# Kernel optimization log

Measured on AMD Instinct MI355X. Metric: run time of the kernel, lower is better.

Reference implementation:

```python
import jax, jax.numpy as jnp
import numpy as np

TEMPERATURE = 0.07
EPS = 1e-12  # F.normalize eps


def _l2norm(x):
    n = jnp.linalg.norm(x, axis=-1, keepdims=True)
    return x / jnp.maximum(n, EPS)


def setup_inputs() -> dict:
    key = jax.random.key(0)
    k1, k2 = jax.random.split(key)
    B, T, H = 16, 512, 1024
    h_source = jax.random.normal(k1, (B, T, H), dtype=jnp.float32)
    h_target = jax.random.normal(k2, (B, T, H), dtype=jnp.float32)
    src_mask = jnp.ones((B, T), dtype=bool)
    tgt_mask = jnp.ones((B, T), dtype=bool)
    return {"h_source": h_source, "h_target": h_target,
            "src_mask": src_mask, "tgt_mask": tgt_mask}


def reference(h_source, h_target, src_mask, tgt_mask):
    # Masks are all-True and B*T == max_samples, so boolean selection == reshape
    # and the random subsampling branch is never taken (deterministic path).
    H = h_source.shape[-1]
    h_s = h_source.reshape(-1, H).astype(jnp.float32)          # (N, H)
    h_t = jax.lax.stop_gradient(h_target.reshape(-1, H)).astype(jnp.float32)  # detached

    h_s_norm = _l2norm(h_s)                                     # (N, H)
    h_t_norm = _l2norm(h_t)                                     # (M, H)
    sim = h_s_norm @ h_t_norm.T                                 # (N, M) cosine sim

    pos_idx = jnp.argmax(sim, axis=1)                           # == topk_idx[:, 0]
    logits = sim / TEMPERATURE
    # cross-entropy with pos_idx labels (stable log-softmax)
    logp = jax.nn.log_softmax(logits, axis=1)
    l_contrastive = -jnp.mean(jnp.take_along_axis(logp, pos_idx[:, None], axis=1)[:, 0])

    # contextual consistency: adjacent source tokens' NN embeddings should align
    nn_embeds = h_t_norm[pos_idx]                               # (N, H)
    nn_sim = jnp.sum(nn_embeds[:-1] * nn_embeds[1:], axis=-1)   # (N-1,)
    l_contextual = 1.0 - jnp.mean(nn_sim)

    return (l_contrastive, l_contextual)
```

## Files before the change

kernel.cpp:

```cpp
#include <hip/hip_runtime.h>
#include <hip/hip_bf16.h>
#include <stdint.h>


#define HDIM 1024
#define NROW 8192
#define TEMP_INV (1.0f / 0.07f)

typedef __attribute__((ext_vector_type(4))) float float4v;
typedef __attribute__((ext_vector_type(2))) float float2v;
typedef __attribute__((ext_vector_type(4))) int   int4v;
typedef __attribute__((ext_vector_type(8))) int   int8v;

#define SN_OFF   ((size_t)0)
#define TN_OFF   ((size_t)8388608)
#define TR_OFF   ((size_t)16777216)
#define SUM_OFF  ((size_t)25165824)
#define PMX_OFF  (SUM_OFF + 32768)
#define ACC_OFF  (PMX_OFF + 65536)
#define CNT_OFF  (ACC_OFF + 64)

static __device__ __forceinline__ void gload_lds16(const void* gptr, void* lptr) {
    __builtin_amdgcn_global_load_lds(
        (const __attribute__((address_space(1))) void*)gptr,
        (__attribute__((address_space(3))) void*)(uintptr_t)(uint32_t)(uintptr_t)lptr,
        16, 0, 0);
}

static __device__ __forceinline__ float fp8dot4(unsigned a, unsigned b) {
    float2v al = __builtin_amdgcn_cvt_pk_f32_fp8((int)a, false);
    float2v ah = __builtin_amdgcn_cvt_pk_f32_fp8((int)a, true);
    float2v bl = __builtin_amdgcn_cvt_pk_f32_fp8((int)b, false);
    float2v bh = __builtin_amdgcn_cvt_pk_f32_fp8((int)b, true);
    return al[0]*bl[0] + al[1]*bl[1] + ah[0]*bh[0] + ah[1]*bh[1];
}

__global__ __launch_bounds__(256)
void norm_kernel(const float* __restrict__ hs, const float* __restrict__ ht,
                 char* __restrict__ Sn, char* __restrict__ Tn, char* __restrict__ Tr,
                 float* __restrict__ sumexp, unsigned long long* __restrict__ pmax,
                 float* __restrict__ acc, unsigned* __restrict__ cnt) {
    const int b = blockIdx.x;
    const int t = threadIdx.x;
    const int wave = t >> 6, lane = t & 63;
    const bool isT = (b >= 512);
    const int g = isT ? (b - 512) : b;
    const float* in = (isT ? ht : hs) + (size_t)g * 16 * HDIM;
    char* outTiled = (isT ? Tn : Sn) + (size_t)g * 16384;

    __shared__ float sq[16][256];
    __shared__ float sscale[16];

    float4v v[16];
    #pragma unroll
    for (int i = 0; i < 16; ++i) {
        v[i] = ((const float4v*)in)[i * 256 + t];
        sq[i][t] = v[i][0]*v[i][0] + v[i][1]*v[i][1] + v[i][2]*v[i][2] + v[i][3]*v[i][3];
    }
    __syncthreads();
    #pragma unroll
    for (int j = 0; j < 4; ++j) {
        const int ri = wave * 4 + j;
        float s = sq[ri][lane] + sq[ri][lane + 64] + sq[ri][lane + 128] + sq[ri][lane + 192];
        #pragma unroll
        for (int off = 1; off < 64; off <<= 1) s += __shfl_xor(s, off);
        if (lane == 0) sscale[ri] = 1.0f / fmaxf(sqrtf(s), 1e-12f);
    }
    __syncthreads();

    char* tiled = (char*)sq;
    const int koff = (t >> 5) * 2048 + ((t >> 2) & 1) * 1024
                   + ((t >> 3) & 3) * 256 + (t & 3) * 4;
    #pragma unroll
    for (int i = 0; i < 16; ++i) {
        const float sc = sscale[i];
        int d = __builtin_amdgcn_cvt_pk_fp8_f32(v[i][0]*sc, v[i][1]*sc, 0, false);
        d     = __builtin_amdgcn_cvt_pk_fp8_f32(v[i][2]*sc, v[i][3]*sc, d, true);
        *(int*)(tiled + koff + i * 16) = d;
        if (isT) ((int*)(Tr + (size_t)(g * 16 + i) * HDIM))[t] = d;
    }
    __syncthreads();
    #pragma unroll
    for (int j = 0; j < 4; ++j)
        ((uint4*)outTiled)[j * 256 + t] = ((const uint4*)tiled)[j * 256 + t];

    if (!isT && t < 16) { sumexp[b * 16 + t] = 0.f; pmax[b * 16 + t] = 0ull; }
    if (b == 0 && t == 16) { acc[0] = 0.f; acc[1] = 0.f; *cnt = 0u; }
}

__global__ __launch_bounds__(256)
__attribute__((amdgpu_waves_per_eu(3, 3)))
void flash_kernel(const char* __restrict__ Sn, const char* __restrict__ Tn,
                  float* __restrict__ sumexp, unsigned long long* __restrict__ pmax) {
    __shared__ float pbSe[128];
    __shared__ unsigned long long pbPk[128];
    const int t = threadIdx.x;
    const int wave = t >> 6, lane = t & 63;
    const int quad = lane >> 4, l16 = lane & 15;

    const int bid = (int)blockIdx.x;
    const int xcd = bid & 7;
    const int idx = bid >> 3;
    const int oct = idx >> 6;
    const int w   = idx & 63;
    const int rbase = (oct * 8 + (w & 7)) * 128;
    const int cbase = (xcd * 8 + (w >> 3)) * 128;

    const int wr = wave & 1, wc = wave >> 1;
    const int wm = wr * 64, wn = wc * 64;

    int vA[4], vB[4];
    #pragma unroll
    for (int u = 0; u < 4; ++u) {
        vA[u] = (rbase / 16 + wr * 4 + u) * 16384 + lane * 16;
        vB[u] = (cbase / 16 + wc * 4 + u) * 16384 + lane * 16;
    }

    float4v acc[4][4];
    #pragma unroll
    for (int i = 0; i < 4; ++i)
        #pragma unroll
        for (int j = 0; j < 4; ++j) acc[i][j] = (float4v){0.f, 0.f, 0.f, 0.f};
    const int usc = 0x7f7f7f7f;

    #pragma unroll 1
    for (int kb = 0; kb < 8; ++kb) {
        int4v alo[4], ahi[4], blo[4], bhi[4];
        #pragma unroll
        for (int u = 0; u < 4; ++u) {
            alo[u] = *(const int4v*)(Sn + vA[u]);
            ahi[u] = *(const int4v*)(Sn + vA[u] + 1024);
        }
        #pragma unroll
        for (int u = 0; u < 4; ++u) {
            blo[u] = *(const int4v*)(Tn + vB[u]);
            bhi[u] = *(const int4v*)(Tn + vB[u] + 1024);
        }
        #pragma unroll
        for (int u = 0; u < 4; ++u) { vA[u] += 2048; vB[u] += 2048; }

        int8v af[4];
        #pragma unroll
        for (int i = 0; i < 4; ++i)
            af[i] = __builtin_shufflevector(alo[i], ahi[i], 0, 1, 2, 3, 4, 5, 6, 7);
        #pragma unroll
        for (int j = 0; j < 4; ++j) {
            int8v bf = __builtin_shufflevector(blo[j], bhi[j], 0, 1, 2, 3, 4, 5, 6, 7);
            #pragma unroll
            for (int i = 0; i < 4; ++i)
                acc[i][j] = __builtin_amdgcn_mfma_scale_f32_16x16x128_f8f6f4(
                    af[i], bf, acc[i][j], 0, 0, 0, usc, 0, usc);
        }
    }

    float se_v[4][4]; unsigned long long pk_v[4][4];
    #pragma unroll
    for (int i = 0; i < 4; ++i) {
        #pragma unroll
        for (int r = 0; r < 4; ++r) {
            float se = 0.f; float mx = -2.f; int mi = 0x7fffffff;
            #pragma unroll
            for (int j = 0; j < 4; ++j) {
                float v = acc[i][j][r];
                se += __expf(v * TEMP_INV);
                int col = cbase + wn + j * 16 + l16;
                if (v > mx || (v == mx && col < mi)) { mx = v; mi = col; }
            }
            #pragma unroll
            for (int off = 1; off < 16; off <<= 1) {
                se += __shfl_xor(se, off);
                float om = __shfl_xor(mx, off);
                int oi = __shfl_xor(mi, off);
                if (om > mx || (om == mx && oi < mi)) { mx = om; mi = oi; }
            }
            se_v[i][r] = se;
            pk_v[i][r] = ((unsigned long long)__float_as_uint(mx + 2.0f) << 32)
                         | (unsigned long long)(0xffffffffu - (unsigned)mi);
        }
    }
    if (wave < 2 && l16 == 0) {
        #pragma unroll
        for (int i = 0; i < 4; ++i)
            #pragma unroll
            for (int r = 0; r < 4; ++r) {
                int rl = wm + i * 16 + quad * 4 + r;
                pbSe[rl] = se_v[i][r]; pbPk[rl] = pk_v[i][r];
            }
    }
    __syncthreads();
    if (wave >= 2 && l16 == 0) {
        #pragma unroll
        for (int i = 0; i < 4; ++i)
            #pragma unroll
            for (int r = 0; r < 4; ++r) {
                int rl = wm + i * 16 + quad * 4 + r;
                float se = se_v[i][r] + pbSe[rl];
                unsigned long long pk = pk_v[i][r];
                unsigned long long po = pbPk[rl];
                if (po > pk) pk = po;
                atomicAdd(&sumexp[rbase + rl], se);
                atomicMax(&pmax[rbase + rl], pk);
            }
    }
}

__global__ __launch_bounds__(256)
void tail_kernel(const float* __restrict__ sumexp,
                 const unsigned long long* __restrict__ pmax,
                 const char* __restrict__ Tr,
                 float* __restrict__ acc, unsigned* __restrict__ cnt,
                 float* __restrict__ out) {
    const int blk = blockIdx.x;
    const int t = threadIdx.x, wave = t >> 6, lane = t & 63;

    if (wave == 0) {
        int r = blk * 32 + (lane & 31);
        unsigned long long p = pmax[r];
        float mx = __uint_as_float((unsigned)(p >> 32)) - 2.0f;
        float loss = logf(sumexp[r]) - mx * TEMP_INV;
        #pragma unroll
        for (int off = 1; off < 32; off <<= 1) loss += __shfl_xor(loss, off);
        if (lane == 0) atomicAdd(acc + 0, loss);
    }

    float s = 0.f;
    #pragma unroll
    for (int it = 0; it < 8; ++it) {
        int g = blk * 32 + wave * 8 + it;
        if (g < NROW - 1) {
            unsigned long long pa = pmax[g], pb = pmax[g + 1];
            int ia = (int)(0xffffffffu - (unsigned)(pa & 0xffffffffu));
            int ib = (int)(0xffffffffu - (unsigned)(pb & 0xffffffffu));
            uint4 va = ((const uint4*)(Tr + (size_t)ia * HDIM))[lane];
            uint4 vb = ((const uint4*)(Tr + (size_t)ib * HDIM))[lane];
            s += fp8dot4(va.x, vb.x) + fp8dot4(va.y, vb.y)
               + fp8dot4(va.z, vb.z) + fp8dot4(va.w, vb.w);
        }
    }
    #pragma unroll
    for (int off = 1; off < 64; off <<= 1) s += __shfl_xor(s, off);
    __shared__ float red[4];
    if (lane == 0) red[wave] = s;
    __syncthreads();
    if (t == 0) atomicAdd(acc + 1, red[0] + red[1] + red[2] + red[3]);

    __threadfence();
    __shared__ unsigned done;
    if (t == 0) done = atomicAdd(cnt, 1u);
    __syncthreads();
    if (t == 0 && done == 255u) {
        float l0 = atomicAdd(acc + 0, 0.0f);
        float l1 = atomicAdd(acc + 1, 0.0f);
        out[0] = l0 / (float)NROW;
        out[1] = 1.0f - l1 / (float)(NROW - 1);
    }
}

extern "C" void kernel_launch(void* const* d_in, const int* in_sizes, int n_in,
                              void* d_out, int out_size, void* d_ws, size_t ws_size,
                              hipStream_t stream) {
    const float* hs = (const float*)d_in[0];
    const float* ht = (const float*)d_in[1];
    char* ws = (char*)d_ws;
    char* Sn = ws + SN_OFF;
    char* Tn = ws + TN_OFF;
    char* Tr = ws + TR_OFF;
    float* sumexp = (float*)(ws + SUM_OFF);
    unsigned long long* pmax = (unsigned long long*)(ws + PMX_OFF);
    float* acc = (float*)(ws + ACC_OFF);
    unsigned* cnt = (unsigned*)(ws + CNT_OFF);
    float* out = (float*)d_out;

    norm_kernel<<<1024, 256, 0, stream>>>(hs, ht, Sn, Tn, Tr, sumexp, pmax, acc, cnt);
    flash_kernel<<<4096, 256, 0, stream>>>(Sn, Tn, sumexp, pmax);
    tail_kernel<<<256, 256, 0, stream>>>(sumexp, pmax, Tr, acc, cnt, out);
}
```

Before: 263.8 us.

## Stage FP8 GEMM operands through double-buffered LDS with async global-to-LDS loads

The flash kernel previously loaded the A and B fp8 tiles straight from global memory into registers on every k-step, and each wave re-read data that other waves also needed. It now copies each k-slab into a double-buffered LDS tile with global_load_lds, prefetching two stages ahead, and feeds the MFMAs from LDS. Barriers and vmcnt waits sequence the buffers, and MFMA issue priority is raised. This cuts redundant global traffic and hides load latency, at the cost of 64KB of LDS per block and occupancy lowered from 3 to 2 waves per EU.

```diff
diff --git a/kernel.cpp b/kernel.cpp
--- a/kernel.cpp
+++ b/kernel.cpp
@@ -89,11 +89,14 @@
 }
 
 __global__ __launch_bounds__(256)
-__attribute__((amdgpu_waves_per_eu(3, 3)))
+__attribute__((amdgpu_waves_per_eu(2, 2)))
 void flash_kernel(const char* __restrict__ Sn, const char* __restrict__ Tn,
                   float* __restrict__ sumexp, unsigned long long* __restrict__ pmax) {
+    __shared__ __align__(16) char As[2][16384];
+    __shared__ __align__(16) char Bs[2][16384];
     __shared__ float pbSe[128];
     __shared__ unsigned long long pbPk[128];
+
     const int t = threadIdx.x;
     const int wave = t >> 6, lane = t & 63;
     const int quad = lane >> 4, l16 = lane & 15;
@@ -109,12 +112,25 @@
     const int wr = wave & 1, wc = wave >> 1;
     const int wm = wr * 64, wn = wc * 64;
 
-    int vA[4], vB[4];
+    int offA[4], offB[4];
     #pragma unroll
     for (int u = 0; u < 4; ++u) {
-        vA[u] = (rbase / 16 + wr * 4 + u) * 16384 + lane * 16;
-        vB[u] = (cbase / 16 + wc * 4 + u) * 16384 + lane * 16;
-    }
+        int ua = wave * 4 + u;
+        offA[u] = (rbase / 16 + (ua >> 1)) * 16384 + (ua & 1) * 1024 + lane * 16;
+        offB[u] = (cbase / 16 + (ua >> 1)) * 16384 + (ua & 1) * 1024 + lane * 16;
+    }
+
+    auto STAGE = [&](int s) {
+        const int ks = s * 2048;
+        char* Ad = As[s & 1];
+        char* Bd = Bs[s & 1];
+        #pragma unroll
+        for (int u = 0; u < 4; ++u)
+            gload_lds16(Sn + offA[u] + ks, Ad + (wave * 4 + u) * 1024);
+        #pragma unroll
+        for (int u = 0; u < 4; ++u)
+            gload_lds16(Tn + offB[u] + ks, Bd + (wave * 4 + u) * 1024);
+    };
 
     float4v acc[4][4];
     #pragma unroll
@@ -123,26 +139,37 @@
         for (int j = 0; j < 4; ++j) acc[i][j] = (float4v){0.f, 0.f, 0.f, 0.f};
     const int usc = 0x7f7f7f7f;
 
+    const int aBase = wr * 4 * 2048 + lane * 16;
+    const int bBase = wc * 4 * 2048 + lane * 16;
+
+    STAGE(0);
+    STAGE(1);
+    asm volatile("s_waitcnt vmcnt(8)\ns_barrier" ::: "memory");
+
     #pragma unroll 1
     for (int kb = 0; kb < 8; ++kb) {
+        const char* Ab = As[kb & 1];
+        const char* Bb = Bs[kb & 1];
+
         int4v alo[4], ahi[4], blo[4], bhi[4];
         #pragma unroll
-        for (int u = 0; u < 4; ++u) {
-            alo[u] = *(const int4v*)(Sn + vA[u]);
-            ahi[u] = *(const int4v*)(Sn + vA[u] + 1024);
-        }
-        #pragma unroll
-        for (int u = 0; u < 4; ++u) {
-            blo[u] = *(const int4v*)(Tn + vB[u]);
-            bhi[u] = *(const int4v*)(Tn + vB[u] + 1024);
-        }
-        #pragma unroll
-        for (int u = 0; u < 4; ++u) { vA[u] += 2048; vB[u] += 2048; }
+        for (int i = 0; i < 4; ++i) {
+            alo[i] = *(const int4v*)(Ab + aBase + i * 2048);
+            ahi[i] = *(const int4v*)(Ab + aBase + i * 2048 + 1024);
+        }
+        #pragma unroll
+        for (int j = 0; j < 4; ++j) {
+            blo[j] = *(const int4v*)(Bb + bBase + j * 2048);
+            bhi[j] = *(const int4v*)(Bb + bBase + j * 2048 + 1024);
+        }
+        asm volatile("s_waitcnt lgkmcnt(0)\ns_barrier" ::: "memory");
+        if (kb < 6) STAGE(kb + 2);
 
         int8v af[4];
         #pragma unroll
         for (int i = 0; i < 4; ++i)
             af[i] = __builtin_shufflevector(alo[i], ahi[i], 0, 1, 2, 3, 4, 5, 6, 7);
+        __builtin_amdgcn_s_setprio(1);
         #pragma unroll
         for (int j = 0; j < 4; ++j) {
             int8v bf = __builtin_shufflevector(blo[j], bhi[j], 0, 1, 2, 3, 4, 5, 6, 7);
@@ -151,6 +178,12 @@
                 acc[i][j] = __builtin_amdgcn_mfma_scale_f32_16x16x128_f8f6f4(
                     af[i], bf, acc[i][j], 0, 0, 0, usc, 0, usc);
         }
+        __builtin_amdgcn_s_setprio(0);
+
+        if (kb < 6)
+            asm volatile("s_waitcnt vmcnt(8)\ns_barrier" ::: "memory");
+        else if (kb == 6)
+            asm volatile("s_waitcnt vmcnt(0)\ns_barrier" ::: "memory");
     }
 
     float se_v[4][4]; unsigned long long pk_v[4][4];
```

Result: slower. 274.6 us (+4.1%).

## Double-buffer B tiles in LDS with async global-to-LDS loads and prefetch A

Applied to the files above, without the earlier changes.

The GEMM main loop of the flash kernel now stages the B (target) fragments into two LDS buffers through global_load_lds, shared across the waves that reuse them. A fragments are prefetched one k-step ahead into registers. Explicit vmcnt waits and barriers, plus raised priority around the MFMA blocks, are meant to overlap the next k-step's memory traffic with the current step's compute and to cut redundant global loads of B. In exchange it adds 32KB of LDS per block, extra barriers, and more register pressure under the fixed 3-waves-per-EU limit.

```diff
diff --git a/kernel.cpp b/kernel.cpp
--- a/kernel.cpp
+++ b/kernel.cpp
@@ -92,8 +92,11 @@
 __attribute__((amdgpu_waves_per_eu(3, 3)))
 void flash_kernel(const char* __restrict__ Sn, const char* __restrict__ Tn,
                   float* __restrict__ sumexp, unsigned long long* __restrict__ pmax) {
+    __shared__ __align__(16) char Bs0[16384];
+    __shared__ __align__(16) char Bs1[16384];
     __shared__ float pbSe[128];
     __shared__ unsigned long long pbPk[128];
+
     const int t = threadIdx.x;
     const int wave = t >> 6, lane = t & 63;
     const int quad = lane >> 4, l16 = lane & 15;
@@ -109,12 +112,32 @@
     const int wr = wave & 1, wc = wave >> 1;
     const int wm = wr * 64, wn = wc * 64;
 
-    int vA[4], vB[4];
+    int offB[4];
     #pragma unroll
     for (int u = 0; u < 4; ++u) {
-        vA[u] = (rbase / 16 + wr * 4 + u) * 16384 + lane * 16;
-        vB[u] = (cbase / 16 + wc * 4 + u) * 16384 + lane * 16;
-    }
+        int ua = wave * 4 + u;
+        offB[u] = (cbase / 16 + (ua >> 1)) * 16384 + (ua & 1) * 1024 + lane * 16;
+    }
+    int vA[4];
+    #pragma unroll
+    for (int i = 0; i < 4; ++i)
+        vA[i] = (rbase / 16 + wr * 4 + i) * 16384 + lane * 16;
+
+    union fragu { int8v v8; int4v v4[2]; };
+    fragu a0[4], a1[4];
+
+    auto STAGE_B = [&](int ks, char* buf) {
+        #pragma unroll
+        for (int u = 0; u < 4; ++u)
+            gload_lds16(Tn + offB[u] + ks, buf + (wave * 4 + u) * 1024);
+    };
+    auto LOAD_A = [&](int ks, fragu* ar) {
+        #pragma unroll
+        for (int i = 0; i < 4; ++i) {
+            ar[i].v4[0] = *(const int4v*)(Sn + vA[i] + ks);
+            ar[i].v4[1] = *(const int4v*)(Sn + vA[i] + ks + 1024);
+        }
+    };
 
     float4v acc[4][4];
     #pragma unroll
@@ -122,34 +145,52 @@
         #pragma unroll
         for (int j = 0; j < 4; ++j) acc[i][j] = (float4v){0.f, 0.f, 0.f, 0.f};
     const int usc = 0x7f7f7f7f;
+    const int bBase = wc * 4 * 2048 + lane * 16;
+
+    STAGE_B(0, Bs0);    LOAD_A(0, a0);
+    STAGE_B(2048, Bs1); LOAD_A(2048, a1);
+    asm volatile("s_waitcnt vmcnt(12)\ns_barrier" ::: "memory");
 
     #pragma unroll 1
-    for (int kb = 0; kb < 8; ++kb) {
-        int4v alo[4], ahi[4], blo[4], bhi[4];
-        #pragma unroll
-        for (int u = 0; u < 4; ++u) {
-            alo[u] = *(const int4v*)(Sn + vA[u]);
-            ahi[u] = *(const int4v*)(Sn + vA[u] + 1024);
-        }
-        #pragma unroll
-        for (int u = 0; u < 4; ++u) {
-            blo[u] = *(const int4v*)(Tn + vB[u]);
-            bhi[u] = *(const int4v*)(Tn + vB[u] + 1024);
-        }
-        #pragma unroll
-        for (int u = 0; u < 4; ++u) { vA[u] += 2048; vB[u] += 2048; }
-
-        int8v af[4];
-        #pragma unroll
-        for (int i = 0; i < 4; ++i)
-            af[i] = __builtin_shufflevector(alo[i], ahi[i], 0, 1, 2, 3, 4, 5, 6, 7);
+    for (int it = 0; it < 4; ++it) {
+        const bool more = (it < 3);
+        const int ks0 = it * 4096 + 4096;
+
+        __builtin_amdgcn_s_setprio(1);
         #pragma unroll
         for (int j = 0; j < 4; ++j) {
-            int8v bf = __builtin_shufflevector(blo[j], bhi[j], 0, 1, 2, 3, 4, 5, 6, 7);
+            fragu bf;
+            bf.v4[0] = *(const int4v*)(Bs0 + bBase + j * 2048);
+            bf.v4[1] = *(const int4v*)(Bs0 + bBase + j * 2048 + 1024);
             #pragma unroll
             for (int i = 0; i < 4; ++i)
                 acc[i][j] = __builtin_amdgcn_mfma_scale_f32_16x16x128_f8f6f4(
-                    af[i], bf, acc[i][j], 0, 0, 0, usc, 0, usc);
+                    a0[i].v8, bf.v8, acc[i][j], 0, 0, 0, usc, 0, usc);
+        }
+        __builtin_amdgcn_s_setprio(0);
+        asm volatile("s_waitcnt lgkmcnt(0)\ns_barrier" ::: "memory");
+        if (more) { STAGE_B(ks0, Bs0); LOAD_A(ks0, a0); }
+        if (more)
+            asm volatile("s_waitcnt vmcnt(12)\ns_barrier" ::: "memory");
+        else
+            asm volatile("s_waitcnt vmcnt(0)\ns_barrier" ::: "memory");
+
+        __builtin_amdgcn_s_setprio(1);
+        #pragma unroll
+        for (int j = 0; j < 4; ++j) {
+            fragu bf;
+            bf.v4[0] = *(const int4v*)(Bs1 + bBase + j * 2048);
+            bf.v4[1] = *(const int4v*)(Bs1 + bBase + j * 2048 + 1024);
+            #pragma unroll
+            for (int i = 0; i < 4; ++i)
+                acc[i][j] = __builtin_amdgcn_mfma_scale_f32_16x16x128_f8f6f4(
+                    a1[i].v8, bf.v8, acc[i][j], 0, 0, 0, usc, 0, usc);
+        }
+        __builtin_amdgcn_s_setprio(0);
+        asm volatile("s_waitcnt lgkmcnt(0)\ns_barrier" ::: "memory");
+        if (more) {
+            STAGE_B(ks0 + 2048, Bs1); LOAD_A(ks0 + 2048, a1);
+            asm volatile("s_waitcnt vmcnt(12)\ns_barrier" ::: "memory");
         }
     }
 
```

New measurement: 745.1 us. 2.82x slower.
